# Kernel optimization log

Hardware: AMD Instinct MI355X
Metric: run time of the kernel (lower is better)

The kernel has to match this reference:

```python
import jax, jax.numpy as jnp
import numpy as np

L = 16384   # sequence length
H = 1024    # feature dim
P = 1024    # state dim (ssm_size=2048, conj_sym=True -> P = ssm_size//2)
STEP_RESCALE = 1.0
CLIP_MAX = -1e-4


def setup_inputs() -> dict:
    key = jax.random.key(0)
    ks = jax.random.split(key, 7)
    log_dt_min, log_dt_max = np.log(0.001), np.log(0.1)
    return {
        "input_sequence": jax.random.normal(ks[0], (L, H), jnp.float32),
        # stable eigenvalues: negative real part
        "Lambda_re": -(jnp.abs(jax.random.normal(ks[1], (P,), jnp.float32)) + 1e-3),
        "Lambda_im": jax.random.normal(ks[2], (P,), jnp.float32) * jnp.pi,
        "B": jax.random.normal(ks[3], (P, H, 2), jnp.float32) / np.sqrt(H),
        "C": jax.random.normal(ks[4], (H, P, 2), jnp.float32) / np.sqrt(P),
        "D": jax.random.normal(ks[5], (H,), jnp.float32),
        "log_step": jax.random.uniform(ks[6], (P, 1), jnp.float32,
                                        minval=log_dt_min, maxval=log_dt_max),
    }


def _binop(q_i, q_j):
    # binary operator of the linear recurrence (diagonal A)
    A_i, b_i = q_i
    A_j, b_j = q_j
    return (A_j * A_i, A_j * b_i + b_j)


def reference(input_sequence, Lambda_re, Lambda_im, B, C, D, log_step):
    # clip_eigs=True: clamp real part at -1e-4
    Lambda = jnp.minimum(Lambda_re, CLIP_MAX) + 1j * Lambda_im        # (P,) complex64
    B_tilde = B[..., 0] + 1j * B[..., 1]                              # (P, H)
    C_tilde = C[..., 0] + 1j * C[..., 1]                              # (H, P)
    step = STEP_RESCALE * jnp.exp(log_step[:, 0])                     # (P,)
    # ZOH discretisation
    Lambda_bar = jnp.exp(Lambda * step)                               # (P,)
    B_bar = ((Lambda_bar - 1.0) / Lambda)[:, None] * B_tilde          # (P, H)
    # input projection: (L,H) @ (H,P) -> (L,P) complex
    Bu = input_sequence.astype(B_bar.dtype) @ B_bar.T
    Lam = jnp.broadcast_to(Lambda_bar, Bu.shape)                      # (L, P)
    # parallel (Blelchley-style) associative scan over time
    _, xs = jax.lax.associative_scan(_binop, (Lam, Bu))               # (L, P)
    # output projection; conj_sym=True -> factor 2 on the real part
    ys = 2.0 * jnp.real(xs @ C_tilde.T)                               # (L, H)
    return ys + input_sequence * D
```

## Files before the change

kernel.cpp:

```cpp
#include <hip/hip_runtime.h>
#include <hip/hip_bf16.h>
#include <stdint.h>


#define L_SEQ 16384
#define H_DIM 1024
#define P_DIM 1024
#define NCH   256
#define TCH   64

typedef __bf16 bf16x8 __attribute__((ext_vector_type(8)));
typedef float  floatx4 __attribute__((ext_vector_type(4)));
using bf16 = __hip_bfloat16;

__device__ __forceinline__ void gld_lds16(const void* g, void* l) {
    __builtin_amdgcn_global_load_lds(
        (const __attribute__((address_space(1))) uint32_t*)g,
        (__attribute__((address_space(3))) uint32_t*)l, 16, 0, 0);
}

__device__ __forceinline__ float lo_bf(uint32_t v) { return __uint_as_float(v << 16); }
__device__ __forceinline__ float hi_bf(uint32_t v) { return __uint_as_float(v & 0xffff0000u); }
__device__ __forceinline__ uint32_t pack_bf(float r, float i) {
    bf16 rb = __float2bfloat16(r), ib = __float2bfloat16(i);
    return ((uint32_t)(*(uint16_t*)&ib) << 16) | (uint32_t)(*(uint16_t*)&rb);
}

__device__ __forceinline__ float rd(const void* p, size_t i, int f) {
    return f ? ((const float*)p)[i]
             : __bfloat162float(((const bf16*)p)[i]);
}

__device__ __forceinline__ int detect_f32(const uint16_t* u) {
    __shared__ int cnt;
    if (threadIdx.x == 0) cnt = 0;
    __syncthreads();
    int c = 0;
    #pragma unroll
    for (int i = 0; i < 8; ++i) {
        int e = (u[threadIdx.x * 8 + i] >> 7) & 0xFF;
        c += (e >= 134);
    }
    if (c) atomicAdd(&cnt, c);
    __syncthreads();
    return cnt > 32;
}

__global__ void convert_u(const void* __restrict__ uin, bf16* __restrict__ ub) {
    const int f = detect_f32((const uint16_t*)uin);
    const size_t g = (size_t)blockIdx.x * 256 + threadIdx.x;
    if (f) {
        const float4* s = (const float4*)uin + g * 2;
        float4 a = s[0], b = s[1];
        alignas(16) bf16 t[8] = {
            __float2bfloat16(a.x), __float2bfloat16(a.y),
            __float2bfloat16(a.z), __float2bfloat16(a.w),
            __float2bfloat16(b.x), __float2bfloat16(b.y),
            __float2bfloat16(b.z), __float2bfloat16(b.w)};
        ((uint4*)ub)[g] = *(const uint4*)t;
    } else {
        ((uint4*)ub)[g] = ((const uint4*)uin)[g];
    }
}

__global__ void prep_all(const void* __restrict__ u,
                         const void* __restrict__ Lre, const void* __restrict__ Lim,
                         const void* __restrict__ lstep, const void* __restrict__ B,
                         const void* __restrict__ C, const void* __restrict__ D,
                         bf16* __restrict__ W1t, bf16* __restrict__ W2t,
                         float* __restrict__ d_f,
                         float2* __restrict__ lam, float2* __restrict__ lamT) {
    const int f = detect_f32((const uint16_t*)u);
    const int p = blockIdx.x;
    float lr = fminf(rd(Lre, p, f), -1e-4f);
    float li = rd(Lim, p, f);
    float s  = expf(rd(lstep, p, f));
    float ea = expf(lr * s);
    float lbr = ea * cosf(li * s), lbi = ea * sinf(li * s);
    float dr = lbr - 1.0f, di = lbi;
    float den = lr * lr + li * li;
    float cr = (dr * lr + di * li) / den;
    float ci = (di * lr - dr * li) / den;
    if (threadIdx.x == 0) {
        lam[p] = make_float2(lbr, lbi);
        float tr = lbr, ti = lbi;
        #pragma unroll
        for (int q = 0; q < 6; ++q) {
            float nr = tr * tr - ti * ti, ni = 2.0f * tr * ti;
            tr = nr; ti = ni;
        }
        lamT[p] = make_float2(tr, ti);
        d_f[p] = rd(D, p, f);
    }
    for (int h = threadIdx.x; h < H_DIM; h += blockDim.x) {
        size_t base = ((size_t)p * H_DIM + h) * 2;
        float br = rd(B, base + 0, f);
        float bi = rd(B, base + 1, f);
        W1t[(size_t)(2 * p)     * H_DIM + h] = __float2bfloat16(cr * br - ci * bi);
        W1t[(size_t)(2 * p + 1) * H_DIM + h] = __float2bfloat16(cr * bi + ci * br);
    }
    const int h = blockIdx.x;
    for (int q = threadIdx.x; q < P_DIM; q += blockDim.x) {
        size_t base = ((size_t)h * P_DIM + q) * 2;
        W2t[(size_t)h * (2 * P_DIM) + 2 * q]     = __float2bfloat16( 2.0f * rd(C, base + 0, f));
        W2t[(size_t)h * (2 * P_DIM) + 2 * q + 1] = __float2bfloat16(-2.0f * rd(C, base + 1, f));
    }
}


#define SB0 __builtin_amdgcn_sched_barrier(0)

#define STAGE(b, t) do {                                                      \
    const int k0_ = (t) * 64;                                                 \
    _Pragma("unroll")                                                         \
    for (int q_ = 0; q_ < 4; ++q_) {                                          \
        const int row_ = q_ * 64 + srow;                                      \
        const int g_   = sg ^ (row_ & 7);                                     \
        gld_lds16(A  + (size_t)(bm + row_) * K + k0_ + g_ * 8,                \
                  sA + (b) * 32768 + q_ * 8192 + wave * 1024);                \
        gld_lds16(Bt + (size_t)(bn + row_) * K + k0_ + g_ * 8,                \
                  sB + (b) * 32768 + q_ * 8192 + wave * 1024);                \
    } } while (0)

#define LDA(b, mh) do {                                                       \
    _Pragma("unroll")                                                         \
    for (int mi_ = 0; mi_ < 4; ++mi_) {                                       \
        const int row_ = wm + ((mh) * 4 + mi_) * 16 + fr;                     \
        _Pragma("unroll")                                                     \
        for (int ks_ = 0; ks_ < 2; ++ks_) {                                   \
            const int ch_ = (ks_ * 4 + kq) ^ (row_ & 7);                      \
            af[mi_][ks_] = *(const bf16x8*)(sA + (b) * 32768 + row_ * 128 + ch_ * 16); \
        } } } while (0)

#define LDB(b, nh) do {                                                       \
    _Pragma("unroll")                                                         \
    for (int ni_ = 0; ni_ < 2; ++ni_) {                                       \
        const int row_ = wn + ((nh) * 2 + ni_) * 16 + fr;                     \
        _Pragma("unroll")                                                     \
        for (int ks_ = 0; ks_ < 2; ++ks_) {                                   \
            const int ch_ = (ks_ * 4 + kq) ^ (row_ & 7);                      \
            bfr[ni_][ks_] = *(const bf16x8*)(sB + (b) * 32768 + row_ * 128 + ch_ * 16); \
        } } } while (0)

#define WAIT_DS do {                                                          \
    asm volatile("s_waitcnt lgkmcnt(0)" ::: "memory");                        \
    SB0;                                                                      \
} while (0)

#define MMA(mh, nh) do {                                                      \
    __builtin_amdgcn_s_setprio(1);                                            \
    _Pragma("unroll")                                                         \
    for (int mi_ = 0; mi_ < 4; ++mi_)                                         \
        _Pragma("unroll")                                                     \
        for (int ni_ = 0; ni_ < 2; ++ni_)                                     \
            _Pragma("unroll")                                                 \
            for (int ks_ = 0; ks_ < 2; ++ks_)                                 \
                acc[(mh) * 4 + mi_][(nh) * 2 + ni_] =                         \
                    __builtin_amdgcn_mfma_f32_16x16x32_bf16(                  \
                        af[mi_][ks_], bfr[ni_][ks_],                          \
                        acc[(mh) * 4 + mi_][(nh) * 2 + ni_], 0, 0, 0);        \
    __builtin_amdgcn_s_setprio(0);                                            \
} while (0)

template <int N, int K, int MODE>
__global__ __launch_bounds__(512, 2) void gemm256(
    const bf16* __restrict__ A, const bf16* __restrict__ Bt,
    bf16* __restrict__ OutBF, float* __restrict__ OutF,
    const bf16* __restrict__ U, const float* __restrict__ Dvec,
    const float2* __restrict__ lam, float2* __restrict__ aggp) {
    constexpr int NXB = N / 256;
    constexpr int KT  = K / 64;
    __shared__ alignas(16) uint8_t sA[2 * 32768];
    __shared__ alignas(16) uint8_t sB[2 * 32768];

    const int tid  = threadIdx.x;
    const int wave = tid >> 6;
    const int lane = tid & 63;
    const int bid  = blockIdx.x;
    const int xr   = bid & 7;
    const int jj   = bid >> 3;
    const int bx   = jj % NXB;
    const int by   = (jj / NXB) * 8 + xr;
    const int bm   = by * 256, bn = bx * 256;
    const int wm   = (wave >> 2) * 128, wn = (wave & 3) * 64;

    floatx4 acc[8][4] = {};

    const int fr   = lane & 15;
    const int kq   = lane >> 4;
    const int srow = tid >> 3;
    const int sg   = tid & 7;

    STAGE(0, 0);
    STAGE(1, 1);
    asm volatile("s_waitcnt vmcnt(8)" ::: "memory");
    SB0;
    __builtin_amdgcn_s_barrier();

    bf16x8 af[4][2], bfr[2][2];

    #pragma unroll 2
    for (int t = 0; t < KT; ++t) {
        const int cur = t & 1;
        LDA(cur, 0); LDB(cur, 0);
        WAIT_DS;
        MMA(0, 0);
        LDB(cur, 1);
        WAIT_DS;
        MMA(0, 1);
        LDA(cur, 1);
        WAIT_DS;
        MMA(1, 1);
        LDB(cur, 0);
        WAIT_DS;
        __builtin_amdgcn_s_barrier();
        if (t + 2 < KT) STAGE(cur, t + 2);
        MMA(1, 0);
        if (t + 2 < KT) {
            asm volatile("s_waitcnt vmcnt(8)" ::: "memory");
        } else {
            asm volatile("s_waitcnt vmcnt(0)" ::: "memory");
        }
        SB0;
        __builtin_amdgcn_s_barrier();
    }

    const int col0  = bn + wn + fr;
    const int rbase = bm + wm + kq * 4;
    #pragma unroll
    for (int mi = 0; mi < 8; ++mi) {
        #pragma unroll
        for (int rr = 0; rr < 4; ++rr) {
            const int row = rbase + mi * 16 + rr;
            #pragma unroll
            for (int ni = 0; ni < 4; ++ni) {
                const int c = col0 + ni * 16;
                float v = acc[mi][ni][rr];
                if (MODE == 2) {
                    float uu = __bfloat162float(U[(size_t)row * H_DIM + c]);
                    __builtin_nontemporal_store(v + uu * Dvec[c],
                                                &OutF[(size_t)row * N + c]);
                } else {
                    OutBF[(size_t)row * N + c] = __float2bfloat16(v);
                }
            }
        }
    }

    if (MODE == 1) {
        const int par = fr & 1;
        const int cg0 = (bm + wm) >> 6;
        #pragma unroll
        for (int ni = 0; ni < 4; ++ni) {
            const int ql = (wn + ni * 16 + (fr & ~1)) >> 1;
            const float2 lb = lam[(bn >> 1) + ql];
            const float l1r = lb.x, l1i = lb.y;
            const float l2r = l1r * l1r - l1i * l1i, l2i = 2.f * l1r * l1i;
            const float l4r = l2r * l2r - l2i * l2i, l4i = 2.f * l2r * l2i;
            const float l8r = l4r * l4r - l4i * l4i, l8i = 2.f * l4r * l4i;
            const float l12r = l8r * l4r - l8i * l4i;
            const float l12i = l8r * l4i + l8i * l4r;
            #pragma unroll
            for (int h = 0; h < 2; ++h) {
                float wr_, wi_;
                if      (kq == 0) { wr_ = l12r; wi_ = l12i; }
                else if (kq == 1) { wr_ = l8r;  wi_ = l8i;  }
                else if (kq == 2) { wr_ = l4r;  wi_ = l4i;  }
                else              { wr_ = 1.f;  wi_ = 0.f;  }
                float s = 0.f;
                #pragma unroll
                for (int mi2 = 3; mi2 >= 0; --mi2) {
                    #pragma unroll
                    for (int rr = 3; rr >= 0; --rr) {
                        float own  = acc[h * 4 + mi2][ni][rr];
                        float part = __shfl_xor(own, 1);
                        s += wr_ * own + (par ? wi_ : -wi_) * part;
                        float nr = wr_ * l1r - wi_ * l1i;
                        float nI = wr_ * l1i + wi_ * l1r;
                        wr_ = nr; wi_ = nI;
                    }
                    float nr = wr_ * l12r - wi_ * l12i;
                    float nI = wr_ * l12i + wi_ * l12r;
                    wr_ = nr; wi_ = nI;
                }
                s += __shfl_xor(s, 16);
                s += __shfl_xor(s, 32);
                float other = __shfl_xor(s, 1);
                if (kq == 0 && par == 0)
                    aggp[(size_t)(cg0 + h) * P_DIM + (bn >> 1) + ql] =
                        make_float2(s, other);
            }
        }
    }
}

__global__ void scan_phase2p(const float2* __restrict__ agg,
                             const float2* __restrict__ lamT,
                             float2* __restrict__ carry) {
    const int w = threadIdx.x >> 6;
    const int j = threadIdx.x & 63;
    const int p = blockIdx.x * 4 + w;
    const float2 A = lamT[p];
    float b2r = A.x * A.x - A.y * A.y, b2i = 2.f * A.x * A.y;
    float Br = b2r * b2r - b2i * b2i, Bi = 2.f * b2r * b2i;
    float2 a[4];
    #pragma unroll
    for (int k = 0; k < 4; ++k) a[k] = agg[(size_t)(4 * j + k) * P_DIM + p];
    float xr = 0.f, xi = 0.f;
    #pragma unroll
    for (int k = 0; k < 4; ++k) {
        float nr = A.x * xr - A.y * xi + a[k].x;
        float ni = A.x * xi + A.y * xr + a[k].y;
        xr = nr; xi = ni;
    }
    float cr = Br, ci = Bi, vr = xr, vi = xi;
    #pragma unroll
    for (int d = 1; d < 64; d <<= 1) {
        float pvr = __shfl_up(vr, d), pvi = __shfl_up(vi, d);
        float pcr = __shfl_up(cr, d), pci = __shfl_up(ci, d);
        if (j >= d) {
            float nvr = cr * pvr - ci * pvi + vr;
            float nvi = cr * pvi + ci * pvr + vi;
            float ncr = cr * pcr - ci * pci;
            float nci = cr * pci + ci * pcr;
            vr = nvr; vi = nvi; cr = ncr; ci = nci;
        }
    }
    float sr = __shfl_up(vr, 1), si = __shfl_up(vi, 1);
    if (j == 0) { sr = 0.f; si = 0.f; }
    #pragma unroll
    for (int k = 0; k < 4; ++k) {
        carry[(size_t)(4 * j + k) * P_DIM + p] = make_float2(sr, si);
        float nr = A.x * sr - A.y * si + a[k].x;
        float ni = A.x * si + A.y * sr + a[k].y;
        sr = nr; si = ni;
    }
}

__global__ void scan_phase3(uint32_t* __restrict__ BuX,
                            const float2* __restrict__ lam,
                            const float2* __restrict__ carry) {
    const int p = blockIdx.y * 256 + threadIdx.x;
    const int c = blockIdx.x;
    const float2 lb = lam[p];
    const float2 c0 = carry[(size_t)c * P_DIM + p];
    float xr = c0.x, xi = c0.y;
    uint32_t* b = BuX + (size_t)c * TCH * P_DIM + p;
    #pragma unroll 4
    for (int j = 0; j < TCH; ++j) {
        uint32_t v = *b;
        float nr = lb.x * xr - lb.y * xi + lo_bf(v);
        float ni = lb.x * xi + lb.y * xr + hi_bf(v);
        xr = nr; xi = ni;
        *b = pack_bf(xr, xi);
        b += P_DIM;
    }
}

extern "C" void kernel_launch(void* const* d_in, const int* in_sizes, int n_in,
                              void* d_out, int out_size, void* d_ws, size_t ws_size,
                              hipStream_t stream) {
    float* out = (float*)d_out;

    char* w = (char*)d_ws;
    w += 256;
    float2* lam   = (float2*)w;  w += (size_t)P_DIM * 8;
    float2* lamT  = (float2*)w;  w += (size_t)P_DIM * 8;
    float*  d_f   = (float*)w;   w += (size_t)H_DIM * 4;
    float2* agg   = (float2*)w;  w += (size_t)NCH * P_DIM * 8;
    float2* carry = (float2*)w;  w += (size_t)NCH * P_DIM * 8;
    bf16*   W1t   = (bf16*)w;    w += (size_t)2 * P_DIM * H_DIM * 2;
    bf16*   W2t   = (bf16*)w;    w += (size_t)H_DIM * 2 * P_DIM * 2;
    bf16*   ub    = (bf16*)w;    w += (size_t)L_SEQ * H_DIM * 2;
    bf16*   Xbuf  = (bf16*)w;

    convert_u<<<(L_SEQ * H_DIM / 8) / 256, 256, 0, stream>>>(d_in[0], ub);
    prep_all<<<P_DIM, 256, 0, stream>>>(d_in[0], d_in[1], d_in[2], d_in[6],
                                        d_in[3], d_in[4], d_in[5],
                                        W1t, W2t, d_f, lam, lamT);

    gemm256<2 * P_DIM, H_DIM, 1><<<(2 * P_DIM / 256) * (L_SEQ / 256), 512, 0, stream>>>(
        ub, W1t, Xbuf, nullptr, nullptr, nullptr, lam, agg);

    scan_phase2p<<<P_DIM / 4, 256, 0, stream>>>(agg, lamT, carry);
    scan_phase3<<<dim3(NCH, P_DIM / 256), 256, 0, stream>>>(
        (uint32_t*)Xbuf, lam, carry);

    gemm256<H_DIM, 2 * P_DIM, 2><<<(H_DIM / 256) * (L_SEQ / 256), 512, 0, stream>>>(
        Xbuf, W2t, nullptr, out, ub, d_f, nullptr, nullptr);
}
```

Baseline: 324.1 us.

## Interleave quarter-tile global-to-LDS staging with MFMA phases in GEMM main loop

Splits each K-tile's global-to-LDS staging into four quarter loads (two halves of A, two of B) and spreads them across the four MFMA phases of the main loop. The next tile's quarters are issued while the current tile's fragments are consumed. The B fragments are now held in two separate register sets, so the second LDB reload is dropped. The aim is a smoother memory/compute overlap with a finer-grained prefetch and lighter vmcnt waits. The cost is extra workgroup barriers per iteration, more registers, and a tighter dependency on LDS buffer reuse order.

```diff
diff --git a/kernel.cpp b/kernel.cpp
--- a/kernel.cpp
+++ b/kernel.cpp
@@ -110,16 +110,18 @@
 
 #define SB0 __builtin_amdgcn_sched_barrier(0)
 
-#define STAGE(b, t) do {                                                      \
+#define STAGEH(b, t, h) do {                                                  \
     const int k0_ = (t) * 64;                                                 \
     _Pragma("unroll")                                                         \
-    for (int q_ = 0; q_ < 4; ++q_) {                                          \
-        const int row_ = q_ * 64 + srow;                                      \
+    for (int q_ = 0; q_ < 2; ++q_) {                                          \
+        const int row_ = ((h) & 1) * 128 + q_ * 64 + srow;                    \
         const int g_   = sg ^ (row_ & 7);                                     \
-        gld_lds16(A  + (size_t)(bm + row_) * K + k0_ + g_ * 8,                \
-                  sA + (b) * 32768 + q_ * 8192 + wave * 1024);                \
-        gld_lds16(Bt + (size_t)(bn + row_) * K + k0_ + g_ * 8,                \
-                  sB + (b) * 32768 + q_ * 8192 + wave * 1024);                \
+        if ((h) < 2)                                                          \
+            gld_lds16(A + (size_t)(bm + row_) * K + k0_ + g_ * 8,             \
+                      sA + (b) * 32768 + ((h) & 1) * 16384 + q_ * 8192 + wave * 1024); \
+        else                                                                  \
+            gld_lds16(Bt + (size_t)(bn + row_) * K + k0_ + g_ * 8,            \
+                      sB + (b) * 32768 + ((h) & 1) * 16384 + q_ * 8192 + wave * 1024); \
     } } while (0)
 
 #define LDA(b, mh) do {                                                       \
@@ -132,14 +134,14 @@
             af[mi_][ks_] = *(const bf16x8*)(sA + (b) * 32768 + row_ * 128 + ch_ * 16); \
         } } } while (0)
 
-#define LDB(b, nh) do {                                                       \
+#define LDB_TO(dst, b, nh) do {                                               \
     _Pragma("unroll")                                                         \
     for (int ni_ = 0; ni_ < 2; ++ni_) {                                       \
         const int row_ = wn + ((nh) * 2 + ni_) * 16 + fr;                     \
         _Pragma("unroll")                                                     \
         for (int ks_ = 0; ks_ < 2; ++ks_) {                                   \
             const int ch_ = (ks_ * 4 + kq) ^ (row_ & 7);                      \
-            bfr[ni_][ks_] = *(const bf16x8*)(sB + (b) * 32768 + row_ * 128 + ch_ * 16); \
+            dst[ni_][ks_] = *(const bf16x8*)(sB + (b) * 32768 + row_ * 128 + ch_ * 16); \
         } } } while (0)
 
 #define WAIT_DS do {                                                          \
@@ -147,7 +149,7 @@
     SB0;                                                                      \
 } while (0)
 
-#define MMA(mh, nh) do {                                                      \
+#define MMA(afv, bfv, mh, nh) do {                                            \
     __builtin_amdgcn_s_setprio(1);                                            \
     _Pragma("unroll")                                                         \
     for (int mi_ = 0; mi_ < 4; ++mi_)                                         \
@@ -157,7 +159,7 @@
             for (int ks_ = 0; ks_ < 2; ++ks_)                                 \
                 acc[(mh) * 4 + mi_][(nh) * 2 + ni_] =                         \
                     __builtin_amdgcn_mfma_f32_16x16x32_bf16(                  \
-                        af[mi_][ks_], bfr[ni_][ks_],                          \
+                        afv[mi_][ks_], bfv[ni_][ks_],                         \
                         acc[(mh) * 4 + mi_][(nh) * 2 + ni_], 0, 0, 0);        \
     __builtin_amdgcn_s_setprio(0);                                            \
 } while (0)
@@ -191,33 +193,41 @@
     const int srow = tid >> 3;
     const int sg   = tid & 7;
 
-    STAGE(0, 0);
-    STAGE(1, 1);
-    asm volatile("s_waitcnt vmcnt(8)" ::: "memory");
+    STAGEH(0, 0, 0); STAGEH(0, 0, 1); STAGEH(0, 0, 2); STAGEH(0, 0, 3);
+    STAGEH(1, 1, 0);
+    asm volatile("s_waitcnt vmcnt(2)" ::: "memory");
     SB0;
     __builtin_amdgcn_s_barrier();
 
-    bf16x8 af[4][2], bfr[2][2];
+    bf16x8 af[4][2], b0[2][2], b1[2][2];
 
     #pragma unroll 2
     for (int t = 0; t < KT; ++t) {
         const int cur = t & 1;
-        LDA(cur, 0); LDB(cur, 0);
+        LDA(cur, 0);
+        LDB_TO(b0, cur, 0);
+        if (t + 1 < KT) STAGEH(cur ^ 1, t + 1, 1);
+        __builtin_amdgcn_s_barrier();
         WAIT_DS;
-        MMA(0, 0);
-        LDB(cur, 1);
+        MMA(af, b0, 0, 0);
+        __builtin_amdgcn_s_barrier();
+        LDB_TO(b1, cur, 1);
+        if (t + 1 < KT) STAGEH(cur ^ 1, t + 1, 2);
+        __builtin_amdgcn_s_barrier();
         WAIT_DS;
-        MMA(0, 1);
+        MMA(af, b1, 0, 1);
+        __builtin_amdgcn_s_barrier();
         LDA(cur, 1);
+        if (t + 1 < KT) STAGEH(cur ^ 1, t + 1, 3);
+        __builtin_amdgcn_s_barrier();
         WAIT_DS;
-        MMA(1, 1);
-        LDB(cur, 0);
-        WAIT_DS;
-        __builtin_amdgcn_s_barrier();
-        if (t + 2 < KT) STAGE(cur, t + 2);
-        MMA(1, 0);
+        MMA(af, b1, 1, 1);
+        __builtin_amdgcn_s_barrier();
+        if (t + 2 < KT) STAGEH(cur, t + 2, 0);
+        __builtin_amdgcn_s_barrier();
+        MMA(af, b0, 1, 0);
         if (t + 2 < KT) {
-            asm volatile("s_waitcnt vmcnt(8)" ::: "memory");
+            asm volatile("s_waitcnt vmcnt(2)" ::: "memory");
         } else {
             asm volatile("s_waitcnt vmcnt(0)" ::: "memory");
         }
```

Measured after the change: 326.6 us. Within noise of the previous version (+0.8%).
